# Optimization experiments

Hardware: AMD Instinct MI355X
Metric: run time of the kernel (lower is better)

## Reference

```python
import jax, jax.numpy as jnp
import numpy as np

K_NEIGHBORS = 16
BN_EPS = 1e-5


def _bn(h, g, b):
    # train-mode BatchNorm1d over (batch, points) per channel, biased variance
    mu = h.mean(axis=(0, 1))
    var = h.var(axis=(0, 1))
    return g * (h - mu) * jax.lax.rsqrt(var + BN_EPS) + b


def _gather(arr, idx):
    # arr: [B,N,D], idx: [B,N,K] -> [B,N,K,D]
    return jax.vmap(lambda a, i: a[i])(arr, idx)


def setup_inputs() -> dict:
    key = jax.random.key(0)
    ks = jax.random.split(key, 16)
    B, N, Cin, C, H, M = 4, 4096, 64, 64, 32, 4
    rn = lambda k, s: jax.random.normal(k, s, dtype=jnp.float32) * 0.05
    return {
        "x": jax.random.normal(ks[0], (B, N, Cin), dtype=jnp.float32),
        "p": jax.random.normal(ks[1], (B, N, 3), dtype=jnp.float32),
        "fc1_w": rn(ks[2], (Cin, C)), "fc1_b": jnp.zeros((C,), jnp.float32),
        "bn1_g": jnp.ones((C,), jnp.float32), "bn1_b": jnp.zeros((C,), jnp.float32),
        "qkv_w": rn(ks[3], (C, 3 * C)),
        "pos_w1": rn(ks[4], (3, H)), "pos_b1": jnp.zeros((H,), jnp.float32),
        "pos_w2": rn(ks[5], (H, C)), "pos_b2": jnp.zeros((C,), jnp.float32),
        "attn_w1": rn(ks[6], (C, M * C)), "attn_b1": jnp.zeros((M * C,), jnp.float32),
        "attn_w2": rn(ks[7], (M * C, C)), "attn_b2": jnp.zeros((C,), jnp.float32),
        "bn2_g": jnp.ones((C,), jnp.float32), "bn2_b": jnp.zeros((C,), jnp.float32),
        "fc2_w": rn(ks[8], (C, C)), "fc2_b": jnp.zeros((C,), jnp.float32),
        "bn3_g": jnp.ones((C,), jnp.float32), "bn3_b": jnp.zeros((C,), jnp.float32),
    }


def reference(x, p, fc1_w, fc1_b, bn1_g, bn1_b, qkv_w,
              pos_w1, pos_b1, pos_w2, pos_b2,
              attn_w1, attn_b1, attn_w2, attn_b2,
              bn2_g, bn2_b, fc2_w, fc2_b, bn3_g, bn3_b):
    C = fc1_w.shape[1]
    # fc1 -> BN -> ReLU
    h = jax.nn.relu(_bn(x @ fc1_w + fc1_b, bn1_g, bn1_b))
    residual = h

    # PointTransformerLayer (vector attention over kNN; mask is all-ones)
    qkv = h @ qkv_w  # [B,N,3C]
    q, k, v = qkv[..., :C], qkv[..., C:2 * C], qkv[..., 2 * C:]
    # squared pairwise distances (matches norm-based topk ranking)
    sq = jnp.sum(p * p, axis=-1)  # [B,N]
    d2 = sq[:, :, None] + sq[:, None, :] - 2.0 * jnp.einsum('bnd,bmd->bnm', p, p)
    _, idx = jax.lax.top_k(-d2, K_NEIGHBORS)  # k smallest distances, [B,N,K]

    kj = _gather(k, idx)          # [B,N,K,C]
    vj = _gather(v, idx)          # [B,N,K,C]
    pj = _gather(p, idx)          # [B,N,K,3]

    rel_pos = p[:, :, None, :] - pj                      # [B,N,K,3]
    pe = jax.nn.relu(rel_pos @ pos_w1 + pos_b1) @ pos_w2 + pos_b2  # [B,N,K,C]

    qk_rel = q[:, :, None, :] - kj                       # [B,N,K,C]
    vv = vj + pe
    sim = jax.nn.relu((qk_rel + pe) @ attn_w1 + attn_b1) @ attn_w2 + attn_b2
    attn = jax.nn.softmax(sim, axis=2)                   # softmax over neighbors
    agg = jnp.sum(attn * vv, axis=2)                     # [B,N,C]

    h2 = jax.nn.relu(_bn(agg, bn2_g, bn2_b))
    y = jax.nn.relu(_bn((h2 + residual) @ fc2_w + fc2_b, bn3_g, bn3_b))
    return (y, p)
```

## Files before the change

kernel.cpp:

```cpp
#include <hip/hip_runtime.h>
#include <math.h>

constexpr int kB = 4, kN = 4096, kK = 16;
constexpr int kRows = kB * kN;
constexpr float kEps = 1e-5f;
constexpr float kFltMax = 3.402823466e38f;
constexpr int kCap = 240;

typedef __attribute__((ext_vector_type(8))) short short8;
typedef __attribute__((ext_vector_type(4))) float f32x4;

__device__ __forceinline__ unsigned short f2bf(float x) {
  return (unsigned short)((__float_as_uint(x) + 0x8000u) >> 16);
}
__device__ __forceinline__ unsigned int pkbf(float lo, float hi) {
  return ((__float_as_uint(lo) + 0x8000u) >> 16) |
         ((__float_as_uint(hi) + 0x8000u) & 0xffff0000u);
}
__device__ __forceinline__ float bflo(unsigned int u) { return __uint_as_float(u << 16); }
__device__ __forceinline__ float bfhi(unsigned int u) { return __uint_as_float(u & 0xffff0000u); }
__device__ __forceinline__ float bfu16(unsigned short us) {
  return __uint_as_float(((unsigned int)us) << 16);
}
__device__ __forceinline__ short8 pack8f(float4 a, float4 b) {
  union { unsigned int u[4]; short8 s; } pk;
  pk.u[0] = pkbf(a.x, a.y);
  pk.u[1] = pkbf(a.z, a.w);
  pk.u[2] = pkbf(b.x, b.y);
  pk.u[3] = pkbf(b.z, b.w);
  return pk.s;
}

__device__ __forceinline__ int lane_prefix(unsigned long long m) {
  return __builtin_amdgcn_mbcnt_hi((unsigned)(m >> 32),
         __builtin_amdgcn_mbcnt_lo((unsigned)m, 0));
}

__device__ __forceinline__ void bitonic64(float& sv, int& si, int lane) {
  #pragma unroll
  for (int k = 2; k <= 64; k <<= 1) {
    #pragma unroll
    for (int j = k >> 1; j > 0; j >>= 1) {
      float ov = __shfl_xor(sv, j);
      int   oi = __shfl_xor(si, j);
      bool up = ((lane & k) == 0);
      bool lower = ((lane & j) == 0);
      bool osm = (ov < sv) || (ov == sv && oi < si);
      bool take = (lower == up) ? osm : !osm;
      if (take) { sv = ov; si = oi; }
    }
  }
}

__device__ __forceinline__ float d2q(const float4& Q, const float4& C) {
  float dt = fmaf(Q.z, C.z, fmaf(Q.y, C.y, Q.x * C.x));
  return fmaf(-2.0f, dt, Q.w + C.w);
}

__global__ void pack_kernel(
    const float* __restrict__ aw1, const float* __restrict__ aw2,
    const float* __restrict__ pw2, const float* __restrict__ qw,
    const float* __restrict__ f2w, const float* __restrict__ f1w,
    const float* __restrict__ pin, float* __restrict__ p4o,
    unsigned short* __restrict__ wpak, float* __restrict__ y) {
  const int id = blockIdx.x * 256 + threadIdx.x;
  if (id < 49152)
    *reinterpret_cast<float4*>(y + 1048576 + 4 * id) =
        *reinterpret_cast<const float4*>(pin + 4 * id);
  if (id < 16384) {
    int j = id & 7, lane = (id >> 3) & 63, rest = id >> 9;
    int mt = rest >> 1, hh = rest & 1;
    wpak[id] = f2bf(aw1[(32 * hh + 8 * (lane >> 4) + j) * 256 + mt * 16 + (lane & 15)]);
    float3 pp = *reinterpret_cast<const float3*>(pin + 3 * id);
    float4 o;
    o.x = pp.x; o.y = pp.y; o.z = pp.z;
    o.w = pp.x * pp.x + pp.y * pp.y + pp.z * pp.z;
    *reinterpret_cast<float4*>(p4o + 4 * id) = o;
  } else if (id < 32768) {
    int i = id - 16384;
    int j = i & 7, lane = (i >> 3) & 63, rest = i >> 9;
    int ct = rest >> 3, f = rest & 7;
    wpak[id] = f2bf(aw2[(32 * f + 8 * (lane >> 4) + j) * 64 + ct * 16 + (lane & 15)]);
  } else if (id < 34816) {
    int i = id - 32768;
    int c = i >> 5, hh = i & 31;
    wpak[id] = f2bf(pw2[hh * 64 + c]);
  } else if (id < 47104) {
    int i = id - 34816;
    int j = i & 7, lane = (i >> 3) & 63, rest = i >> 9;
    int ct = rest >> 1, hh = rest & 1;
    wpak[id] = f2bf(qw[(32 * hh + 8 * (lane >> 4) + j) * 192 + ct * 16 + (lane & 15)]);
  } else if (id < 51200) {
    int i = id - 47104;
    int j = i & 7, lane = (i >> 3) & 63, rest = i >> 9;
    int ct = rest >> 1, hh = rest & 1;
    wpak[id] = f2bf(f2w[(32 * hh + 8 * (lane >> 4) + j) * 64 + ct * 16 + (lane & 15)]);
  } else if (id < 55296) {
    int i = id - 51200;
    int j = i & 7, lane = (i >> 3) & 63, rest = i >> 9;
    int ct = rest >> 1, hh = rest & 1;
    wpak[id] = f2bf(f1w[(32 * hh + 8 * (lane >> 4) + j) * 64 + ct * 16 + (lane & 15)]);
  }
}

__global__ __launch_bounds__(256) void fc1_conv_kernel(
    const float* __restrict__ x, const unsigned short* __restrict__ f1wf,
    const float* __restrict__ bias, float* __restrict__ out,
    float* __restrict__ part) {
  __shared__ float SS[4][4][16], SS2[4][4][16];
  const int t = threadIdx.x;
  const int blk = blockIdx.x;
  const int lane = t & 63, wv = t >> 6;
  const int l = lane & 15, q = lane >> 4;
  const int r0 = blk * 64;
  const int row = r0 + wv * 16 + l;
  const f32x4 zero = {0.f, 0.f, 0.f, 0.f};
  float4 xa0 = *reinterpret_cast<const float4*>(&x[row * 64 + q * 8]);
  float4 xa1 = *reinterpret_cast<const float4*>(&x[row * 64 + q * 8 + 4]);
  float4 xb0 = *reinterpret_cast<const float4*>(&x[row * 64 + 32 + q * 8]);
  float4 xb1 = *reinterpret_cast<const float4*>(&x[row * 64 + 32 + q * 8 + 4]);
  short8 a0 = pack8f(xa0, xa1), a1 = pack8f(xb0, xb1);
  #pragma unroll
  for (int ct = 0; ct < 4; ++ct) {
    short8 b0 = *reinterpret_cast<const short8*>(&f1wf[(ct * 2 + 0) * 512 + lane * 8]);
    short8 b1 = *reinterpret_cast<const short8*>(&f1wf[(ct * 2 + 1) * 512 + lane * 8]);
    f32x4 acc = __builtin_amdgcn_mfma_f32_16x16x32_bf16(a0, b0, zero, 0, 0, 0);
    acc = __builtin_amdgcn_mfma_f32_16x16x32_bf16(a1, b1, acc, 0, 0, 0);
    const float bc = bias[ct * 16 + l];
    float s = 0.f, s2 = 0.f;
    #pragma unroll
    for (int i = 0; i < 4; ++i) {
      float v = acc[i] + bc;
      out[(r0 + wv * 16 + q * 4 + i) * 64 + ct * 16 + l] = v;
      s += v; s2 += v * v;
    }
    s  += __shfl_xor(s, 16, 64);  s  += __shfl_xor(s, 32, 64);
    s2 += __shfl_xor(s2, 16, 64); s2 += __shfl_xor(s2, 32, 64);
    if (q == 0) { SS[wv][ct][l] = s; SS2[wv][ct][l] = s2; }
  }
  __syncthreads();
  if (t < 64) {
    int ct = t >> 4, lc = t & 15;
    part[blk * 128 + t] = SS[0][ct][lc] + SS[1][ct][lc] + SS[2][ct][lc] + SS[3][ct][lc];
    part[blk * 128 + 64 + t] =
        SS2[0][ct][lc] + SS2[1][ct][lc] + SS2[2][ct][lc] + SS2[3][ct][lc];
  }
}

__global__ void stats_part_kernel(const float* __restrict__ src, float* __restrict__ part) {
  __shared__ float sb[256], sb2[256];
  const int t = threadIdx.x, blk = blockIdx.x;
  const int c = t & 63, rg = t >> 6;
  float s = 0.f, s2 = 0.f;
  for (int r = rg; r < 64; r += 4) {
    float v = src[(blk * 64 + r) * 64 + c];
    s += v; s2 += v * v;
  }
  sb[t] = s; sb2[t] = s2; __syncthreads();
  if (t < 64) {
    float ts  = sb[t] + sb[64 + t] + sb[128 + t] + sb[192 + t];
    float ts2 = sb2[t] + sb2[64 + t] + sb2[128 + t] + sb2[192 + t];
    part[blk * 128 + t] = ts;
    part[blk * 128 + 64 + t] = ts2;
  }
}

__global__ __launch_bounds__(1024) void stats_fin_kernel(
    const float* __restrict__ part,
    const float* __restrict__ g, const float* __restrict__ b,
    float* __restrict__ A, float* __restrict__ Bv, int cnt) {
  __shared__ double ds[1024], ds2[1024];
  const int t = threadIdx.x;
  const int c = t & 63, grp = t >> 6;
  const int per = cnt >> 4;
  double s = 0.0, s2 = 0.0;
  for (int k = 0; k < per; ++k) {
    int i = grp * per + k;
    s  += part[i * 128 + c];
    s2 += part[i * 128 + 64 + c];
  }
  ds[grp * 64 + c] = s; ds2[grp * 64 + c] = s2;
  __syncthreads();
  if (t < 64) {
    double ts = 0.0, ts2 = 0.0;
    #pragma unroll
    for (int gg = 0; gg < 16; ++gg) { ts += ds[gg * 64 + t]; ts2 += ds2[gg * 64 + t]; }
    double mean = ts / (double)kRows;
    double var = ts2 / (double)kRows - mean * mean;
    float rs = (float)(1.0 / sqrt(var + (double)kEps));
    float Af = g[t] * rs;
    A[t] = Af;
    Bv[t] = b[t] - (float)mean * Af;
  }
}

__global__ __launch_bounds__(256) void qkv_bn_kernel(
    const float* __restrict__ hpre, const float* __restrict__ A1,
    const float* __restrict__ B1, const unsigned short* __restrict__ wqf,
    float* __restrict__ hout, unsigned short* __restrict__ out) {
  const int t = threadIdx.x, lane = t & 63, wv = t >> 6;
  const int l = lane & 15, q = lane >> 4;
  const int r0 = blockIdx.x * 64;
  const int row = r0 + wv * 16 + l;
  const f32x4 zero = {0.f, 0.f, 0.f, 0.f};
  short8 af[2];
  #pragma unroll
  for (int hh = 0; hh < 2; ++hh) {
    const int c0 = 32 * hh + q * 8;
    float4 v0 = *reinterpret_cast<const float4*>(&hpre[row * 64 + c0]);
    float4 v1 = *reinterpret_cast<const float4*>(&hpre[row * 64 + c0 + 4]);
    float4 Aa = *reinterpret_cast<const float4*>(&A1[c0]);
    float4 Ab = *reinterpret_cast<const float4*>(&A1[c0 + 4]);
    float4 Ba = *reinterpret_cast<const float4*>(&B1[c0]);
    float4 Bb = *reinterpret_cast<const float4*>(&B1[c0 + 4]);
    v0.x = fmaxf(Aa.x * v0.x + Ba.x, 0.f); v0.y = fmaxf(Aa.y * v0.y + Ba.y, 0.f);
    v0.z = fmaxf(Aa.z * v0.z + Ba.z, 0.f); v0.w = fmaxf(Aa.w * v0.w + Ba.w, 0.f);
    v1.x = fmaxf(Ab.x * v1.x + Bb.x, 0.f); v1.y = fmaxf(Ab.y * v1.y + Bb.y, 0.f);
    v1.z = fmaxf(Ab.z * v1.z + Bb.z, 0.f); v1.w = fmaxf(Ab.w * v1.w + Bb.w, 0.f);
    *reinterpret_cast<float4*>(&hout[row * 64 + c0]) = v0;
    *reinterpret_cast<float4*>(&hout[row * 64 + c0 + 4]) = v1;
    af[hh] = pack8f(v0, v1);
  }
  #pragma unroll
  for (int ct = 0; ct < 12; ++ct) {
    short8 b0 = *reinterpret_cast<const short8*>(&wqf[((ct * 2 + 0) * 64 + lane) * 8]);
    short8 b1 = *reinterpret_cast<const short8*>(&wqf[((ct * 2 + 1) * 64 + lane) * 8]);
    f32x4 acc = __builtin_amdgcn_mfma_f32_16x16x32_bf16(af[0], b0, zero, 0, 0, 0);
    acc = __builtin_amdgcn_mfma_f32_16x16x32_bf16(af[1], b1, acc, 0, 0, 0);
    #pragma unroll
    for (int i = 0; i < 4; ++i)
      out[(r0 + wv * 16 + q * 4 + i) * 192 + ct * 16 + l] = f2bf(acc[i]);
  }
}

__global__ __launch_bounds__(256, 4) void knn_attn_kernel(
    const float* __restrict__ p4, const unsigned short* __restrict__ qkv,
    const float* __restrict__ pos_w1, const float* __restrict__ pos_b1,
    const float* __restrict__ pos_b2,
    const float* __restrict__ attn_b1, const float* __restrict__ attn_b2,
    const unsigned short* __restrict__ w1f,
    const unsigned short* __restrict__ w2f,
    const unsigned short* __restrict__ pw2t,
    float* __restrict__ agg) {
  __shared__ unsigned short Ulds[64 * 72];
  __shared__ unsigned short VVb[64 * 72];
  __shared__ float sthr[4];
  __shared__ int   scnt[4];

  const int t = threadIdx.x;
  const int lane = t & 63, w = t >> 6;
  const int l = lane & 15, q = lane >> 4;
  const int work = ((blockIdx.x & 7) << 9) | (blockIdx.x >> 3);
  const int b = work >> 10;
  const int pt_row = work * 4 + w;
  const int qrow0 = work * 4;
  const int base = b * kN;
  const f32x4 zero = {0.f, 0.f, 0.f, 0.f};

  if (t < 4) scnt[t] = 0;

  const float4 q0f = *reinterpret_cast<const float4*>(p4 + 4 * (qrow0 + 0));
  const float4 q1f = *reinterpret_cast<const float4*>(p4 + 4 * (qrow0 + 1));
  const float4 q2f = *reinterpret_cast<const float4*>(p4 + 4 * (qrow0 + 2));
  const float4 q3f = *reinterpret_cast<const float4*>(p4 + 4 * (qrow0 + 3));
  const float4 qp4 = *reinterpret_cast<const float4*>(p4 + 4 * pt_row);
  const float qx = qp4.x, qy = qp4.y, qz = qp4.z, sqq = qp4.w;

  unsigned pk0[8], pk1[8], pk2[8], pk3[8];
  float lmin = kFltMax;
  const int cbase = base + w * 1024;
  #pragma unroll
  for (int g = 0; g < 2; ++g) {
    float4 cc[8];
    #pragma unroll
    for (int jj = 0; jj < 8; ++jj)
      cc[jj] = *reinterpret_cast<const float4*>(p4 + 4 * (cbase + (g * 8 + jj) * 64 + lane));
    #pragma unroll
    for (int jj = 0; jj < 8; ++jj) {
      float dot = fmaf(qz, cc[jj].z, fmaf(qy, cc[jj].y, qx * cc[jj].x));
      lmin = fminf(lmin, fmaf(-2.0f, dot, sqq + cc[jj].w));
    }
    #pragma unroll
    for (int pi = 0; pi < 4; ++pi) {
      const float4 ca = cc[2 * pi], cb = cc[2 * pi + 1];
      pk0[g * 4 + pi] = (__float_as_uint(d2q(q0f, ca)) >> 16) |
                        (__float_as_uint(d2q(q0f, cb)) & 0xffff0000u);
      pk1[g * 4 + pi] = (__float_as_uint(d2q(q1f, ca)) >> 16) |
                        (__float_as_uint(d2q(q1f, cb)) & 0xffff0000u);
      pk2[g * 4 + pi] = (__float_as_uint(d2q(q2f, ca)) >> 16) |
                        (__float_as_uint(d2q(q2f, cb)) & 0xffff0000u);
      pk3[g * 4 + pi] = (__float_as_uint(d2q(q3f, ca)) >> 16) |
                        (__float_as_uint(d2q(q3f, cb)) & 0xffff0000u);
    }
  }
  {
    int dummy = lane;
    float lm = lmin;
    bitonic64(lm, dummy, lane);
    float s16 = __shfl(lm, 15);
    if (lane == 0) sthr[w] = s16 + 1e-3f;
  }
  __syncthreads();

  {
    auto append_q = [&](const unsigned (&PK)[8], int j) {
      int* listj = reinterpret_cast<int*>(VVb) + j * 576;
      const float thrj = sthr[j];
      #pragma unroll
      for (int g = 0; g < 2; ++g) {
        unsigned long long m[8];
        int pc[8];
        #pragma unroll
        for (int c = 0; c < 8; ++c) {
          unsigned pku = PK[g * 4 + (c >> 1)];
          float dv = (c & 1) ? __uint_as_float(pku & 0xffff0000u)
                             : __uint_as_float(pku << 16);
          m[c] = __ballot(dv <= thrj);
          pc[c] = __popcll(m[c]);
        }
        int tot = pc[0] + pc[1] + pc[2] + pc[3] + pc[4] + pc[5] + pc[6] + pc[7];
        int old = 0;
        if (lane == 0) old = atomicAdd(&scnt[j], tot);
        old = __shfl(old, 0);
        int pre = 0;
        #pragma unroll
        for (int c = 0; c < 8; ++c) {
          if ((m[c] >> lane) & 1ull) {
            int pos = old + pre + lane_prefix(m[c]);
            if (pos < kCap) listj[pos] = w * 1024 + (g * 8 + c) * 64 + lane;
          }
          pre += pc[c];
        }
      }
    };
    append_q(pk0, 0);
    append_q(pk1, 1);
    append_q(pk2, 2);
    append_q(pk3, 3);
  }
  __syncthreads();

  const int n = scnt[w];
  const int* bufi = reinterpret_cast<const int*>(VVb) + w * 576;
  float sv = kFltMax;
  int   si = 0x7fffffff;
  if (n <= kCap) {
    for (int g0 = 0; g0 < n; g0 += 48) {
      float mv; int mi;
      if (lane < 16) { mv = sv; mi = si; }
      else {
        int pos = g0 + (lane - 16);
        if (pos < n) {
          int jj = bufi[pos];
          float4 c = *reinterpret_cast<const float4*>(p4 + 4 * (base + jj));
          mv = d2q(qp4, c);
          mi = jj;
        } else { mv = kFltMax; mi = 0x7fffffff; }
      }
      bitonic64(mv, mi, lane);
      sv = mv; si = mi;
    }
  } else {
    for (int g0 = 0; g0 < kN; g0 += 48) {
      float mv; int mi;
      if (lane < 16) { mv = sv; mi = si; }
      else {
        int j = g0 + (lane - 16);
        if (j < kN) {
          float4 c = *reinterpret_cast<const float4*>(p4 + 4 * (base + j));
          mv = d2q(qp4, c);
          mi = j;
        } else { mv = kFltMax; mi = 0x7fffffff; }
      }
      bitonic64(mv, mi, lane);
      sv = mv; si = mi;
    }
  }

  int idxv = 0;
  if (lane < 16) {
    int o = si;
    if ((unsigned)o >= (unsigned)kN) o = 0;
    idxv = o;
  }

  asm volatile("" ::: "memory");

  {
    const int r = lane >> 2, seg = lane & 3;
    const unsigned short* jrow = qkv + (base + __shfl(idxv, r)) * 192;
    const int c0 = seg * 16;
    uint4 k0 = *reinterpret_cast<const uint4*>(jrow + 64 + c0);
    uint4 k1 = *reinterpret_cast<const uint4*>(jrow + 64 + c0 + 8);
    uint4 v0 = *reinterpret_cast<const uint4*>(jrow + 128 + c0);
    uint4 v1 = *reinterpret_cast<const uint4*>(jrow + 128 + c0 + 8);
    uint4 q0 = *reinterpret_cast<const uint4*>(qkv + pt_row * 192 + c0);
    uint4 q1 = *reinterpret_cast<const uint4*>(qkv + pt_row * 192 + c0 + 8);
    auto diff2 = [](unsigned int qu, unsigned int ku) -> unsigned int {
      float lo = bflo(qu) - bflo(ku);
      float hi = bfhi(qu) - bfhi(ku);
      return pkbf(lo, hi);
    };
    uint4 u0, u1;
    u0.x = diff2(q0.x, k0.x); u0.y = diff2(q0.y, k0.y);
    u0.z = diff2(q0.z, k0.z); u0.w = diff2(q0.w, k0.w);
    u1.x = diff2(q1.x, k1.x); u1.y = diff2(q1.y, k1.y);
    u1.z = diff2(q1.z, k1.z); u1.w = diff2(q1.w, k1.w);
    *reinterpret_cast<uint4*>(&Ulds[(w * 16 + r) * 72 + c0]) = u0;
    *reinterpret_cast<uint4*>(&Ulds[(w * 16 + r) * 72 + c0 + 8]) = u1;
    *reinterpret_cast<uint4*>(&VVb[(w * 16 + r) * 72 + c0]) = v0;
    *reinterpret_cast<uint4*>(&VVb[(w * 16 + r) * 72 + c0 + 8]) = v1;
  }
  short8 pbf;
  {
    const int nj = __shfl(idxv, l);
    const float4 pj4 = *reinterpret_cast<const float4*>(p4 + 4 * (base + nj));
    float rx = qx - pj4.x, ry = qy - pj4.y, rz = qz - pj4.z;
    float hv[8];
    #pragma unroll
    for (int j = 0; j < 8; ++j) {
      int hh = q * 8 + j;
      hv[j] = fmaxf(pos_b1[hh] + rx * pos_w1[hh] + ry * pos_w1[32 + hh] +
                    rz * pos_w1[64 + hh], 0.0f);
    }
    union { unsigned int u[4]; short8 s; } pk;
    #pragma unroll
    for (int ii = 0; ii < 4; ++ii) pk.u[ii] = pkbf(hv[2 * ii], hv[2 * ii + 1]);
    pbf = pk.s;
  }

  {
    const int urow = (w * 16 + l) * 72;
    #pragma unroll
    for (int mt = 0; mt < 4; ++mt) {
      short8 paf = *reinterpret_cast<const short8*>(&pw2t[(mt * 16 + l) * 32 + q * 8]);
      f32x4 pe = __builtin_amdgcn_mfma_f32_16x16x32_bf16(paf, pbf, zero, 0, 0, 0);
      const int c0 = mt * 16 + q * 4;
      float4 b2v = *reinterpret_cast<const float4*>(&pos_b2[c0]);
      float pe0 = pe[0] + b2v.x, pe1 = pe[1] + b2v.y;
      float pe2 = pe[2] + b2v.z, pe3 = pe[3] + b2v.w;
      uint2 u2 = *reinterpret_cast<uint2*>(&Ulds[urow + c0]);
      uint2 o;
      o.x = pkbf(bflo(u2.x) + pe0, bfhi(u2.x) + pe1);
      o.y = pkbf(bflo(u2.y) + pe2, bfhi(u2.y) + pe3);
      *reinterpret_cast<uint2*>(&Ulds[urow + c0]) = o;
      uint2 v2 = *reinterpret_cast<uint2*>(&VVb[urow + c0]);
      uint2 ov;
      ov.x = pkbf(bflo(v2.x) + pe0, bfhi(v2.x) + pe1);
      ov.y = pkbf(bflo(v2.y) + pe2, bfhi(v2.y) + pe3);
      *reinterpret_cast<uint2*>(&VVb[urow + c0]) = ov;
    }
  }

  {
    f32x4 acc2[4];
    #pragma unroll
    for (int ct = 0; ct < 4; ++ct) acc2[ct] = zero;
    const int urow = (w * 16 + l) * 72;
    short8 ub0 = *reinterpret_cast<const short8*>(&Ulds[urow + q * 8]);
    short8 ub1 = *reinterpret_cast<const short8*>(&Ulds[urow + 32 + q * 8]);
    const int sbase = l + 32 * (q & 1);
    const bool hi_mt = (q >= 2);
    #pragma unroll
    for (int f = 0; f < 8; ++f) {
      unsigned plo2[2], phi2[2];
      #pragma unroll
      for (int s = 0; s < 2; ++s) {
        const int mt = 2 * f + s;
        short8 a0 = *reinterpret_cast<const short8*>(&w1f[(mt * 2 + 0) * 512 + lane * 8]);
        short8 a1 = *reinterpret_cast<const short8*>(&w1f[(mt * 2 + 1) * 512 + lane * 8]);
        f32x4 acc = __builtin_amdgcn_mfma_f32_16x16x32_bf16(a0, ub0, zero, 0, 0, 0);
        acc = __builtin_amdgcn_mfma_f32_16x16x32_bf16(a1, ub1, acc, 0, 0, 0);
        float4 bb = *reinterpret_cast<const float4*>(&attn_b1[mt * 16 + q * 4]);
        plo2[s] = pkbf(fmaxf(acc[0] + bb.x, 0.f), fmaxf(acc[1] + bb.y, 0.f));
        phi2[s] = pkbf(fmaxf(acc[2] + bb.z, 0.f), fmaxf(acc[3] + bb.w, 0.f));
      }
      union { unsigned int u[4]; short8 s; } pk;
      #pragma unroll
      for (int d = 0; d < 4; ++d) {
        const int src = sbase + ((d >> 1) << 4);
        const unsigned int w0 = (d & 1) ? phi2[0] : plo2[0];
        const unsigned int w1v = (d & 1) ? phi2[1] : plo2[1];
        unsigned int va = (unsigned int)__shfl((int)w0, src);
        unsigned int vb = (unsigned int)__shfl((int)w1v, src);
        pk.u[d] = hi_mt ? vb : va;
      }
      short8 afr = pk.s;
      #pragma unroll
      for (int ct = 0; ct < 4; ++ct) {
        short8 bfr = *reinterpret_cast<const short8*>(&w2f[((ct * 8 + f) * 64 + lane) * 8]);
        acc2[ct] = __builtin_amdgcn_mfma_f32_16x16x32_bf16(afr, bfr, acc2[ct], 0, 0, 0);
      }
    }
    #pragma unroll
    for (int ct = 0; ct < 4; ++ct) {
      const int ch = ct * 16 + l;
      const float bv = attn_b2[ch];
      float s0v = acc2[ct][0] + bv, s1v = acc2[ct][1] + bv;
      float s2v = acc2[ct][2] + bv, s3v = acc2[ct][3] + bv;
      float mx = fmaxf(fmaxf(s0v, s1v), fmaxf(s2v, s3v));
      mx = fmaxf(mx, __shfl_xor(mx, 16, 64));
      mx = fmaxf(mx, __shfl_xor(mx, 32, 64));
      float e0 = __expf(s0v - mx), e1 = __expf(s1v - mx);
      float e2 = __expf(s2v - mx), e3 = __expf(s3v - mx);
      float se = e0 + e1 + e2 + e3;
      se += __shfl_xor(se, 16, 64);
      se += __shfl_xor(se, 32, 64);
      const int vbase = (w * 16 + q * 4) * 72 + ch;
      float a = e0 * bfu16(VVb[vbase])       + e1 * bfu16(VVb[vbase + 72]) +
                e2 * bfu16(VVb[vbase + 144]) + e3 * bfu16(VVb[vbase + 216]);
      a += __shfl_xor(a, 16, 64);
      a += __shfl_xor(a, 32, 64);
      if (q == 0) agg[pt_row * 64 + ch] = a / se;
    }
  }
}

__global__ __launch_bounds__(256) void fc2_mfma_kernel(
    const float* __restrict__ aggp, const float* __restrict__ hres,
    const float* __restrict__ A2, const float* __restrict__ B2,
    const unsigned short* __restrict__ fc2f, const float* __restrict__ bias,
    float* __restrict__ z, float* __restrict__ part) {
  __shared__ float SS[4][4][16], SS2[4][4][16];
  const int t = threadIdx.x, lane = t & 63, wv = t >> 6;
  const int l = lane & 15, q = lane >> 4;
  const int r0 = blockIdx.x * 64;
  const int row = r0 + wv * 16 + l;
  const f32x4 zero = {0.f, 0.f, 0.f, 0.f};
  short8 af[2];
  #pragma unroll
  for (int hh = 0; hh < 2; ++hh) {
    const int c0 = 32 * hh + q * 8;
    float4 v0 = *reinterpret_cast<const float4*>(&aggp[row * 64 + c0]);
    float4 v1 = *reinterpret_cast<const float4*>(&aggp[row * 64 + c0 + 4]);
    float4 r0v = *reinterpret_cast<const float4*>(&hres[row * 64 + c0]);
    float4 r1v = *reinterpret_cast<const float4*>(&hres[row * 64 + c0 + 4]);
    float4 Aa = *reinterpret_cast<const float4*>(&A2[c0]);
    float4 Ab = *reinterpret_cast<const float4*>(&A2[c0 + 4]);
    float4 Ba = *reinterpret_cast<const float4*>(&B2[c0]);
    float4 Bb = *reinterpret_cast<const float4*>(&B2[c0 + 4]);
    v0.x = fmaxf(Aa.x * v0.x + Ba.x, 0.f) + r0v.x;
    v0.y = fmaxf(Aa.y * v0.y + Ba.y, 0.f) + r0v.y;
    v0.z = fmaxf(Aa.z * v0.z + Ba.z, 0.f) + r0v.z;
    v0.w = fmaxf(Aa.w * v0.w + Ba.w, 0.f) + r0v.w;
    v1.x = fmaxf(Ab.x * v1.x + Bb.x, 0.f) + r1v.x;
    v1.y = fmaxf(Ab.y * v1.y + Bb.y, 0.f) + r1v.y;
    v1.z = fmaxf(Ab.z * v1.z + Bb.z, 0.f) + r1v.z;
    v1.w = fmaxf(Ab.w * v1.w + Bb.w, 0.f) + r1v.w;
    af[hh] = pack8f(v0, v1);
  }
  #pragma unroll
  for (int ct = 0; ct < 4; ++ct) {
    short8 b0 = *reinterpret_cast<const short8*>(&fc2f[((ct * 2 + 0) * 64 + lane) * 8]);
    short8 b1 = *reinterpret_cast<const short8*>(&fc2f[((ct * 2 + 1) * 64 + lane) * 8]);
    f32x4 acc = __builtin_amdgcn_mfma_f32_16x16x32_bf16(af[0], b0, zero, 0, 0, 0);
    acc = __builtin_amdgcn_mfma_f32_16x16x32_bf16(af[1], b1, acc, 0, 0, 0);
    const float bc = bias[ct * 16 + l];
    float s = 0.f, s2 = 0.f;
    #pragma unroll
    for (int i = 0; i < 4; ++i) {
      float v = acc[i] + bc;
      z[(r0 + wv * 16 + q * 4 + i) * 64 + ct * 16 + l] = v;
      s += v; s2 += v * v;
    }
    s  += __shfl_xor(s, 16, 64);  s  += __shfl_xor(s, 32, 64);
    s2 += __shfl_xor(s2, 16, 64); s2 += __shfl_xor(s2, 32, 64);
    if (q == 0) { SS[wv][ct][l] = s; SS2[wv][ct][l] = s2; }
  }
  __syncthreads();
  if (t < 64) {
    int ct = t >> 4, lc = t & 15;
    part[blockIdx.x * 128 + t] =
        SS[0][ct][lc] + SS[1][ct][lc] + SS[2][ct][lc] + SS[3][ct][lc];
    part[blockIdx.x * 128 + 64 + t] =
        SS2[0][ct][lc] + SS2[1][ct][lc] + SS2[2][ct][lc] + SS2[3][ct][lc];
  }
}

__global__ void final_kernel(const float* __restrict__ z, const float* __restrict__ A3,
                             const float* __restrict__ B3, float* __restrict__ y) {
  const int i = blockIdx.x * 256 + threadIdx.x;
  const int c = i & 63;
  y[i] = fmaxf(A3[c] * z[i] + B3[c], 0.0f);
}

extern "C" void kernel_launch(void* const* d_in, const int* in_sizes, int n_in,
                              void* d_out, int out_size, void* d_ws, size_t ws_size,
                              hipStream_t stream) {
  const float* x       = (const float*)d_in[0];
  const float* p       = (const float*)d_in[1];
  const float* fc1_w   = (const float*)d_in[2];
  const float* fc1_b   = (const float*)d_in[3];
  const float* bn1_g   = (const float*)d_in[4];
  const float* bn1_b   = (const float*)d_in[5];
  const float* qkv_w   = (const float*)d_in[6];
  const float* pos_w1  = (const float*)d_in[7];
  const float* pos_b1  = (const float*)d_in[8];
  const float* pos_w2  = (const float*)d_in[9];
  const float* pos_b2  = (const float*)d_in[10];
  const float* attn_w1 = (const float*)d_in[11];
  const float* attn_b1 = (const float*)d_in[12];
  const float* attn_w2 = (const float*)d_in[13];
  const float* attn_b2 = (const float*)d_in[14];
  const float* bn2_g   = (const float*)d_in[15];
  const float* bn2_b   = (const float*)d_in[16];
  const float* fc2_w   = (const float*)d_in[17];
  const float* fc2_b   = (const float*)d_in[18];
  const float* bn3_g   = (const float*)d_in[19];
  const float* bn3_b   = (const float*)d_in[20];

  float* ws   = (float*)d_ws;
  float* h    = ws;
  unsigned short* qkvb = (unsigned short*)(ws + 1048576);
  float* hpre = ws + 4194304;
  float* aggv = ws + 5242880;
  float* z    = ws + 6291456;
  float* st   = ws + 7340032;
  float* p4   = ws + 7356800;
  unsigned short* wpak = (unsigned short*)(ws + 7618944);
  unsigned short* w1f  = wpak;
  unsigned short* w2f  = wpak + 16384;
  unsigned short* pw2t = wpak + 32768;
  unsigned short* wqf  = wpak + 34816;
  unsigned short* fc2f = wpak + 47104;
  unsigned short* f1wf = wpak + 51200;

  float* A1 = st,       *B1 = st + 64;
  float* A2 = st + 128, *B2 = st + 192;
  float* A3 = st + 256, *B3 = st + 320;
  float* y = (float*)d_out;

  pack_kernel<<<216, 256, 0, stream>>>(attn_w1, attn_w2, pos_w2, qkv_w, fc2_w,
                                       fc1_w, p, p4, wpak, y);
  fc1_conv_kernel<<<256, 256, 0, stream>>>(x, f1wf, fc1_b, hpre, aggv);
  stats_fin_kernel<<<1, 1024, 0, stream>>>(aggv, bn1_g, bn1_b, A1, B1, 256);
  qkv_bn_kernel<<<256, 256, 0, stream>>>(hpre, A1, B1, wqf, h, qkvb);
  knn_attn_kernel<<<4096, 256, 0, stream>>>(p4, qkvb, pos_w1, pos_b1, pos_b2,
                                            attn_b1, attn_b2, w1f, w2f, pw2t, aggv);
  stats_part_kernel<<<256, 256, 0, stream>>>(aggv, z);
  stats_fin_kernel<<<1, 1024, 0, stream>>>(z, bn2_g, bn2_b, A2, B2, 256);
  fc2_mfma_kernel<<<256, 256, 0, stream>>>(aggv, h, A2, B2, fc2f, fc2_b, z, hpre);
  stats_fin_kernel<<<1, 1024, 0, stream>>>(hpre, bn3_g, bn3_b, A3, B3, 256);
  final_kernel<<<4096, 256, 0, stream>>>(z, A3, B3, y);
}
```

Baseline: 243.2 us.

## Fuse BN stat kernels into producers via grid-wide last-block barriers

Replaces separate stats/finalize/apply kernel launches with in-kernel grid synchronization. The last-arriving block computes the BatchNorm scale and shift while the other blocks spin on a flag. This merges fc1 with qkv and folds the BN2/fc2/BN3/final stages into one kernel, keeping intermediates in LDS or registers instead of round-tripping through global memory. It relies on all 256 blocks being co-resident, otherwise the spin-wait deadlocks, and it adds atomic and fence overhead.

```diff
diff --git a/kernel.cpp b/kernel.cpp
--- a/kernel.cpp
+++ b/kernel.cpp
@@ -57,13 +57,69 @@
   return fmaf(-2.0f, dt, Q.w + C.w);
 }
 
+__device__ __forceinline__ bool arrive_last(int* counter, int nblk) {
+  __shared__ int lastf;
+  __syncthreads();
+  __threadfence();
+  if (threadIdx.x == 0) {
+    int old = __hip_atomic_fetch_add(counter, 1, __ATOMIC_ACQ_REL,
+                                     __HIP_MEMORY_SCOPE_AGENT);
+    lastf = (old == nblk - 1) ? 1 : 0;
+  }
+  __syncthreads();
+  return lastf != 0;
+}
+__device__ __forceinline__ void set_flag(int* flag) {
+  __threadfence();
+  __syncthreads();
+  if (threadIdx.x == 0)
+    __hip_atomic_store(flag, 1, __ATOMIC_RELEASE, __HIP_MEMORY_SCOPE_AGENT);
+}
+__device__ __forceinline__ void wait_flag(int* flag) {
+  if (threadIdx.x == 0) {
+    while (__hip_atomic_load(flag, __ATOMIC_ACQUIRE,
+                             __HIP_MEMORY_SCOPE_AGENT) == 0)
+      __builtin_amdgcn_s_sleep(2);
+  }
+  __syncthreads();
+}
+
+__device__ void fin_compute(const float* __restrict__ part,
+                            const float* __restrict__ g,
+                            const float* __restrict__ b,
+                            float* __restrict__ A, float* __restrict__ Bv) {
+  __shared__ double fd[256], fd2[256];
+  const int t = threadIdx.x, c = t & 63, grp = t >> 6;
+  double s = 0.0, s2 = 0.0;
+  for (int k = 0; k < 64; ++k) {
+    int i = grp * 64 + k;
+    s  += part[i * 128 + c];
+    s2 += part[i * 128 + 64 + c];
+  }
+  fd[grp * 64 + c] = s; fd2[grp * 64 + c] = s2;
+  __syncthreads();
+  if (t < 64) {
+    double ts  = fd[t] + fd[64 + t] + fd[128 + t] + fd[192 + t];
+    double ts2 = fd2[t] + fd2[64 + t] + fd2[128 + t] + fd2[192 + t];
+    double mean = ts / (double)kRows;
+    double var = ts2 / (double)kRows - mean * mean;
+    float rs = (float)(1.0 / sqrt(var + (double)kEps));
+    float Af = g[t] * rs;
+    A[t] = Af;
+    Bv[t] = b[t] - (float)mean * Af;
+  }
+  __syncthreads();
+}
+
 __global__ void pack_kernel(
     const float* __restrict__ aw1, const float* __restrict__ aw2,
     const float* __restrict__ pw2, const float* __restrict__ qw,
     const float* __restrict__ f2w, const float* __restrict__ f1w,
     const float* __restrict__ pin, float* __restrict__ p4o,
-    unsigned short* __restrict__ wpak, float* __restrict__ y) {
+    unsigned short* __restrict__ wpak, float* __restrict__ y,
+    int* __restrict__ syncbuf) {
   const int id = blockIdx.x * 256 + threadIdx.x;
+  if (id < 8) syncbuf[id] = 0;
   if (id < 49152)
     *reinterpret_cast<float4*>(y + 1048576 + 4 * id) =
         *reinterpret_cast<const float4*>(pin + 4 * id);
@@ -103,10 +159,15 @@
   }
 }
 
-__global__ __launch_bounds__(256) void fc1_conv_kernel(
+__global__ __launch_bounds__(256, 4) void fc1_qkv_kernel(
     const float* __restrict__ x, const unsigned short* __restrict__ f1wf,
-    const float* __restrict__ bias, float* __restrict__ out,
-    float* __restrict__ part) {
+    const float* __restrict__ fc1_b,
+    const float* __restrict__ bn1_g, const float* __restrict__ bn1_b,
+    const unsigned short* __restrict__ wqf,
+    float* __restrict__ part, float* __restrict__ A1, float* __restrict__ B1,
+    int* __restrict__ counter, int* __restrict__ flag,
+    float* __restrict__ hout, unsigned short* __restrict__ qkvb) {
+  __shared__ float H[64][68];
   __shared__ float SS[4][4][16], SS2[4][4][16];
   const int t = threadIdx.x;
   const int blk = blockIdx.x;
@@ -115,28 +176,30 @@
   const int r0 = blk * 64;
   const int row = r0 + wv * 16 + l;
   const f32x4 zero = {0.f, 0.f, 0.f, 0.f};
-  float4 xa0 = *reinterpret_cast<const float4*>(&x[row * 64 + q * 8]);
-  float4 xa1 = *reinterpret_cast<const float4*>(&x[row * 64 + q * 8 + 4]);
-  float4 xb0 = *reinterpret_cast<const float4*>(&x[row * 64 + 32 + q * 8]);
-  float4 xb1 = *reinterpret_cast<const float4*>(&x[row * 64 + 32 + q * 8 + 4]);
-  short8 a0 = pack8f(xa0, xa1), a1 = pack8f(xb0, xb1);
-  #pragma unroll
-  for (int ct = 0; ct < 4; ++ct) {
-    short8 b0 = *reinterpret_cast<const short8*>(&f1wf[(ct * 2 + 0) * 512 + lane * 8]);
-    short8 b1 = *reinterpret_cast<const short8*>(&f1wf[(ct * 2 + 1) * 512 + lane * 8]);
-    f32x4 acc = __builtin_amdgcn_mfma_f32_16x16x32_bf16(a0, b0, zero, 0, 0, 0);
-    acc = __builtin_amdgcn_mfma_f32_16x16x32_bf16(a1, b1, acc, 0, 0, 0);
-    const float bc = bias[ct * 16 + l];
-    float s = 0.f, s2 = 0.f;
-    #pragma unroll
-    for (int i = 0; i < 4; ++i) {
-      float v = acc[i] + bc;
-      out[(r0 + wv * 16 + q * 4 + i) * 64 + ct * 16 + l] = v;
-      s += v; s2 += v * v;
-    }
-    s  += __shfl_xor(s, 16, 64);  s  += __shfl_xor(s, 32, 64);
-    s2 += __shfl_xor(s2, 16, 64); s2 += __shfl_xor(s2, 32, 64);
-    if (q == 0) { SS[wv][ct][l] = s; SS2[wv][ct][l] = s2; }
+  {
+    float4 xa0 = *reinterpret_cast<const float4*>(&x[row * 64 + q * 8]);
+    float4 xa1 = *reinterpret_cast<const float4*>(&x[row * 64 + q * 8 + 4]);
+    float4 xb0 = *reinterpret_cast<const float4*>(&x[row * 64 + 32 + q * 8]);
+    float4 xb1 = *reinterpret_cast<const float4*>(&x[row * 64 + 32 + q * 8 + 4]);
+    short8 a0 = pack8f(xa0, xa1), a1 = pack8f(xb0, xb1);
+    #pragma unroll
+    for (int ct = 0; ct < 4; ++ct) {
+      short8 b0 = *reinterpret_cast<const short8*>(&f1wf[(ct * 2 + 0) * 512 + lane * 8]);
+      short8 b1 = *reinterpret_cast<const short8*>(&f1wf[(ct * 2 + 1) * 512 + lane * 8]);
+      f32x4 acc = __builtin_amdgcn_mfma_f32_16x16x32_bf16(a0, b0, zero, 0, 0, 0);
+      acc = __builtin_amdgcn_mfma_f32_16x16x32_bf16(a1, b1, acc, 0, 0, 0);
+      const float bc = fc1_b[ct * 16 + l];
+      float s = 0.f, s2 = 0.f;
+      #pragma unroll
+      for (int i = 0; i < 4; ++i) {
+        float v = acc[i] + bc;
+        H[wv * 16 + q * 4 + i][ct * 16 + l] = v;
+        s += v; s2 += v * v;
+      }
+      s  += __shfl_xor(s, 16, 64);  s  += __shfl_xor(s, 32, 64);
+      s2 += __shfl_xor(s2, 16, 64); s2 += __shfl_xor(s2, 32, 64);
+      if (q == 0) { SS[wv][ct][l] = s; SS2[wv][ct][l] = s2; }
+    }
   }
   __syncthreads();
   if (t < 64) {
@@ -145,91 +208,43 @@
     part[blk * 128 + 64 + t] =
         SS2[0][ct][lc] + SS2[1][ct][lc] + SS2[2][ct][lc] + SS2[3][ct][lc];
   }
-}
-
-__global__ void stats_part_kernel(const float* __restrict__ src, float* __restrict__ part) {
-  __shared__ float sb[256], sb2[256];
-  const int t = threadIdx.x, blk = blockIdx.x;
-  const int c = t & 63, rg = t >> 6;
-  float s = 0.f, s2 = 0.f;
-  for (int r = rg; r < 64; r += 4) {
-    float v = src[(blk * 64 + r) * 64 + c];
-    s += v; s2 += v * v;
-  }
-  sb[t] = s; sb2[t] = s2; __syncthreads();
-  if (t < 64) {
-    float ts  = sb[t] + sb[64 + t] + sb[128 + t] + sb[192 + t];
-    float ts2 = sb2[t] + sb2[64 + t] + sb2[128 + t] + sb2[192 + t];
-    part[blk * 128 + t] = ts;
-    part[blk * 128 + 64 + t] = ts2;
-  }
-}
-
-__global__ __launch_bounds__(1024) void stats_fin_kernel(
-    const float* __restrict__ part,
-    const float* __restrict__ g, const float* __restrict__ b,
-    float* __restrict__ A, float* __restrict__ Bv, int cnt) {
-  __shared__ double ds[1024], ds2[1024];
-  const int t = threadIdx.x;
-  const int c = t & 63, grp = t >> 6;
-  const int per = cnt >> 4;
-  double s = 0.0, s2 = 0.0;
-  for (int k = 0; k < per; ++k) {
-    int i = grp * per + k;
-    s  += part[i * 128 + c];
-    s2 += part[i * 128 + 64 + c];
-  }
-  ds[grp * 64 + c] = s; ds2[grp * 64 + c] = s2;
-  __syncthreads();
-  if (t < 64) {
-    double ts = 0.0, ts2 = 0.0;
-    #pragma unroll
-    for (int gg = 0; gg < 16; ++gg) { ts += ds[gg * 64 + t]; ts2 += ds2[gg * 64 + t]; }
-    double mean = ts / (double)kRows;
-    double var = ts2 / (double)kRows - mean * mean;
-    float rs = (float)(1.0 / sqrt(var + (double)kEps));
-    float Af = g[t] * rs;
-    A[t] = Af;
-    Bv[t] = b[t] - (float)mean * Af;
-  }
-}
-
-__global__ __launch_bounds__(256) void qkv_bn_kernel(
-    const float* __restrict__ hpre, const float* __restrict__ A1,
-    const float* __restrict__ B1, const unsigned short* __restrict__ wqf,
-    float* __restrict__ hout, unsigned short* __restrict__ out) {
-  const int t = threadIdx.x, lane = t & 63, wv = t >> 6;
-  const int l = lane & 15, q = lane >> 4;
-  const int r0 = blockIdx.x * 64;
-  const int row = r0 + wv * 16 + l;
-  const f32x4 zero = {0.f, 0.f, 0.f, 0.f};
-  short8 af[2];
-  #pragma unroll
-  for (int hh = 0; hh < 2; ++hh) {
-    const int c0 = 32 * hh + q * 8;
-    float4 v0 = *reinterpret_cast<const float4*>(&hpre[row * 64 + c0]);
-    float4 v1 = *reinterpret_cast<const float4*>(&hpre[row * 64 + c0 + 4]);
-    float4 Aa = *reinterpret_cast<const float4*>(&A1[c0]);
-    float4 Ab = *reinterpret_cast<const float4*>(&A1[c0 + 4]);
-    float4 Ba = *reinterpret_cast<const float4*>(&B1[c0]);
-    float4 Bb = *reinterpret_cast<const float4*>(&B1[c0 + 4]);
-    v0.x = fmaxf(Aa.x * v0.x + Ba.x, 0.f); v0.y = fmaxf(Aa.y * v0.y + Ba.y, 0.f);
-    v0.z = fmaxf(Aa.z * v0.z + Ba.z, 0.f); v0.w = fmaxf(Aa.w * v0.w + Ba.w, 0.f);
-    v1.x = fmaxf(Ab.x * v1.x + Bb.x, 0.f); v1.y = fmaxf(Ab.y * v1.y + Bb.y, 0.f);
-    v1.z = fmaxf(Ab.z * v1.z + Bb.z, 0.f); v1.w = fmaxf(Ab.w * v1.w + Bb.w, 0.f);
-    *reinterpret_cast<float4*>(&hout[row * 64 + c0]) = v0;
-    *reinterpret_cast<float4*>(&hout[row * 64 + c0 + 4]) = v1;
-    af[hh] = pack8f(v0, v1);
-  }
-  #pragma unroll
-  for (int ct = 0; ct < 12; ++ct) {
-    short8 b0 = *reinterpret_cast<const short8*>(&wqf[((ct * 2 + 0) * 64 + lane) * 8]);
-    short8 b1 = *reinterpret_cast<const short8*>(&wqf[((ct * 2 + 1) * 64 + lane) * 8]);
-    f32x4 acc = __builtin_amdgcn_mfma_f32_16x16x32_bf16(af[0], b0, zero, 0, 0, 0);
-    acc = __builtin_amdgcn_mfma_f32_16x16x32_bf16(af[1], b1, acc, 0, 0, 0);
-    #pragma unroll
-    for (int i = 0; i < 4; ++i)
-      out[(r0 + wv * 16 + q * 4 + i) * 192 + ct * 16 + l] = f2bf(acc[i]);
+  if (arrive_last(counter, 256)) {
+    __threadfence();
+    fin_compute(part, bn1_g, bn1_b, A1, B1);
+    set_flag(flag);
+  } else {
+    wait_flag(flag);
+  }
+  __threadfence();
+  {
+    short8 af[2];
+    #pragma unroll
+    for (int hh = 0; hh < 2; ++hh) {
+      const int c0 = 32 * hh + q * 8;
+      float4 v0 = *reinterpret_cast<const float4*>(&H[wv * 16 + l][c0]);
+      float4 v1 = *reinterpret_cast<const float4*>(&H[wv * 16 + l][c0 + 4]);
+      float4 Aa = *reinterpret_cast<const float4*>(&A1[c0]);
+      float4 Ab = *reinterpret_cast<const float4*>(&A1[c0 + 4]);
+      float4 Ba = *reinterpret_cast<const float4*>(&B1[c0]);
+      float4 Bb = *reinterpret_cast<const float4*>(&B1[c0 + 4]);
+      v0.x = fmaxf(Aa.x * v0.x + Ba.x, 0.f); v0.y = fmaxf(Aa.y * v0.y + Ba.y, 0.f);
+      v0.z = fmaxf(Aa.z * v0.z + Ba.z, 0.f); v0.w = fmaxf(Aa.w * v0.w + Ba.w, 0.f);
+      v1.x = fmaxf(Ab.x * v1.x + Bb.x, 0.f); v1.y = fmaxf(Ab.y * v1.y + Bb.y, 0.f);
+      v1.z = fmaxf(Ab.z * v1.z + Bb.z, 0.f); v1.w = fmaxf(Ab.w * v1.w + Bb.w, 0.f);
+      *reinterpret_cast<float4*>(&hout[row * 64 + c0]) = v0;
+      *reinterpret_cast<float4*>(&hout[row * 64 + c0 + 4]) = v1;
+      af[hh] = pack8f(v0, v1);
+    }
+    #pragma unroll
+    for (int ct = 0; ct < 12; ++ct) {
+      short8 b0 = *reinterpret_cast<const short8*>(&wqf[((ct * 2 + 0) * 64 + lane) * 8]);
+      short8 b1 = *reinterpret_cast<const short8*>(&wqf[((ct * 2 + 1) * 64 + lane) * 8]);
+      f32x4 acc = __builtin_amdgcn_mfma_f32_16x16x32_bf16(af[0], b0, zero, 0, 0, 0);
+      acc = __builtin_amdgcn_mfma_f32_16x16x32_bf16(af[1], b1, acc, 0, 0, 0);
+      #pragma unroll
+      for (int i = 0; i < 4; ++i)
+        qkvb[(r0 + wv * 16 + q * 4 + i) * 192 + ct * 16 + l] = f2bf(acc[i]);
+    }
   }
 }
 
@@ -516,72 +531,172 @@
   }
 }
 
-__global__ __launch_bounds__(256) void fc2_mfma_kernel(
+__global__ __launch_bounds__(256, 4) void fc2_final_kernel(
     const float* __restrict__ aggp, const float* __restrict__ hres,
-    const float* __restrict__ A2, const float* __restrict__ B2,
-    const unsigned short* __restrict__ fc2f, const float* __restrict__ bias,
-    float* __restrict__ z, float* __restrict__ part) {
+    const float* __restrict__ bn2_g, const float* __restrict__ bn2_b,
+    const float* __restrict__ bn3_g, const float* __restrict__ bn3_b,
+    const unsigned short* __restrict__ fc2f, const float* __restrict__ fc2_b,
+    float* __restrict__ partA, float* __restrict__ partZ,
+    float* __restrict__ A2, float* __restrict__ B2,
+    float* __restrict__ A3, float* __restrict__ B3,
+    int* __restrict__ counter2, int* __restrict__ flag2,
+    int* __restrict__ counter3, int* __restrict__ flag3,
+    float* __restrict__ y) {
   __shared__ float SS[4][4][16], SS2[4][4][16];
   const int t = threadIdx.x, lane = t & 63, wv = t >> 6;
   const int l = lane & 15, q = lane >> 4;
   const int r0 = blockIdx.x * 64;
   const int row = r0 + wv * 16 + l;
   const f32x4 zero = {0.f, 0.f, 0.f, 0.f};
-  short8 af[2];
-  #pragma unroll
-  for (int hh = 0; hh < 2; ++hh) {
-    const int c0 = 32 * hh + q * 8;
-    float4 v0 = *reinterpret_cast<const float4*>(&aggp[row * 64 + c0]);
-    float4 v1 = *reinterpret_cast<const float4*>(&aggp[row * 64 + c0 + 4]);
-    float4 r0v = *reinterpret_cast<const float4*>(&hres[row * 64 + c0]);
-    float4 r1v = *reinterpret_cast<const float4*>(&hres[row * 64 + c0 + 4]);
-    float4 Aa = *reinterpret_cast<const float4*>(&A2[c0]);
-    float4 Ab = *reinterpret_cast<const float4*>(&A2[c0 + 4]);
-    float4 Ba = *reinterpret_cast<const float4*>(&B2[c0]);
-    float4 Bb = *reinterpret_cast<const float4*>(&B2[c0 + 4]);
-    v0.x = fmaxf(Aa.x * v0.x + Ba.x, 0.f) + r0v.x;
-    v0.y = fmaxf(Aa.y * v0.y + Ba.y, 0.f) + r0v.y;
-    v0.z = fmaxf(Aa.z * v0.z + Ba.z, 0.f) + r0v.z;
-    v0.w = fmaxf(Aa.w * v0.w + Ba.w, 0.f) + r0v.w;
-    v1.x = fmaxf(Ab.x * v1.x + Bb.x, 0.f) + r1v.x;
-    v1.y = fmaxf(Ab.y * v1.y + Bb.y, 0.f) + r1v.y;
-    v1.z = fmaxf(Ab.z * v1.z + Bb.z, 0.f) + r1v.z;
-    v1.w = fmaxf(Ab.w * v1.w + Bb.w, 0.f) + r1v.w;
-    af[hh] = pack8f(v0, v1);
-  }
+  float4 g0 = *reinterpret_cast<const float4*>(&aggp[row * 64 + q * 8]);
+  float4 g1 = *reinterpret_cast<const float4*>(&aggp[row * 64 + q * 8 + 4]);
+  float4 g2 = *reinterpret_cast<const float4*>(&aggp[row * 64 + 32 + q * 8]);
+  float4 g3 = *reinterpret_cast<const float4*>(&aggp[row * 64 + 32 + q * 8 + 4]);
+  float4 r0v = *reinterpret_cast<const float4*>(&hres[row * 64 + q * 8]);
+  float4 r1v = *reinterpret_cast<const float4*>(&hres[row * 64 + q * 8 + 4]);
+  float4 r2v = *reinterpret_cast<const float4*>(&hres[row * 64 + 32 + q * 8]);
+  float4 r3v = *reinterpret_cast<const float4*>(&hres[row * 64 + 32 + q * 8 + 4]);
+  {
+    float sv[8], s2v[8];
+    const float gg[8] = {g0.x, g0.y, g0.z, g0.w, g1.x, g1.y, g1.z, g1.w};
+    const float hh2[8] = {g2.x, g2.y, g2.z, g2.w, g3.x, g3.y, g3.z, g3.w};
+    #pragma unroll
+    for (int j = 0; j < 8; ++j) { sv[j] = gg[j]; s2v[j] = gg[j] * gg[j]; }
+    #pragma unroll
+    for (int st = 1; st < 16; st <<= 1) {
+      #pragma unroll
+      for (int j = 0; j < 8; ++j) {
+        sv[j]  += __shfl_xor(sv[j], st, 64);
+        s2v[j] += __shfl_xor(s2v[j], st, 64);
+      }
+    }
+    if (l == 0) {
+      #pragma unroll
+      for (int j = 0; j < 8; ++j) {
+        SS[wv][0][q * 4 + (j >> 1)] = 0.f;
+      }
+    }
+    if (l == 0) {
+      #pragma unroll
+      for (int j = 0; j < 8; ++j) {
+        (&SS[wv][0][0])[q * 8 + j]  = sv[j];
+        (&SS2[wv][0][0])[q * 8 + j] = s2v[j];
+      }
+    }
+    #pragma unroll
+    for (int j = 0; j < 8; ++j) { sv[j] = hh2[j]; s2v[j] = hh2[j] * hh2[j]; }
+    #pragma unroll
+    for (int st = 1; st < 16; st <<= 1) {
+      #pragma unroll
+      for (int j = 0; j < 8; ++j) {
+        sv[j]  += __shfl_xor(sv[j], st, 64);
+        s2v[j] += __shfl_xor(s2v[j], st, 64);
+      }
+    }
+    if (l == 0) {
+      #pragma unroll
+      for (int j = 0; j < 8; ++j) {
+        (&SS[wv][0][0])[32 + q * 8 + j]  = sv[j];
+        (&SS2[wv][0][0])[32 + q * 8 + j] = s2v[j];
+      }
+    }
+  }
+  __syncthreads();
+  if (t < 64) {
+    partA[blockIdx.x * 128 + t] = (&SS[0][0][0])[t] + (&SS[1][0][0])[t] +
+                                  (&SS[2][0][0])[t] + (&SS[3][0][0])[t];
+    partA[blockIdx.x * 128 + 64 + t] = (&SS2[0][0][0])[t] + (&SS2[1][0][0])[t] +
+                                       (&SS2[2][0][0])[t] + (&SS2[3][0][0])[t];
+  }
+  if (arrive_last(counter2, 256)) {
+    __threadfence();
+    fin_compute(partA, bn2_g, bn2_b, A2, B2);
+    set_flag(flag2);
+  } else {
+    wait_flag(flag2);
+  }
+  __threadfence();
+  float zv[4][4];
+  {
+    short8 af[2];
+    {
+      const int c0 = q * 8;
+      float4 Aa = *reinterpret_cast<const float4*>(&A2[c0]);
+      float4 Ab = *reinterpret_cast<const float4*>(&A2[c0 + 4]);
+      float4 Ba = *reinterpret_cast<const float4*>(&B2[c0]);
+      float4 Bb = *reinterpret_cast<const float4*>(&B2[c0 + 4]);
+      float4 v0 = g0, v1 = g1;
+      v0.x = fmaxf(Aa.x * v0.x + Ba.x, 0.f) + r0v.x;
+      v0.y = fmaxf(Aa.y * v0.y + Ba.y, 0.f) + r0v.y;
+      v0.z = fmaxf(Aa.z * v0.z + Ba.z, 0.f) + r0v.z;
+      v0.w = fmaxf(Aa.w * v0.w + Ba.w, 0.f) + r0v.w;
+      v1.x = fmaxf(Ab.x * v1.x + Bb.x, 0.f) + r1v.x;
+      v1.y = fmaxf(Ab.y * v1.y + Bb.y, 0.f) + r1v.y;
+      v1.z = fmaxf(Ab.z * v1.z + Bb.z, 0.f) + r1v.z;
+      v1.w = fmaxf(Ab.w * v1.w + Bb.w, 0.f) + r1v.w;
+      af[0] = pack8f(v0, v1);
+    }
+    {
+      const int c0 = 32 + q * 8;
+      float4 Aa = *reinterpret_cast<const float4*>(&A2[c0]);
+      float4 Ab = *reinterpret_cast<const float4*>(&A2[c0 + 4]);
+      float4 Ba = *reinterpret_cast<const float4*>(&B2[c0]);
+      float4 Bb = *reinterpret_cast<const float4*>(&B2[c0 + 4]);
+      float4 v0 = g2, v1 = g3;
+      v0.x = fmaxf(Aa.x * v0.x + Ba.x, 0.f) + r2v.x;
+      v0.y = fmaxf(Aa.y * v0.y + Ba.y, 0.f) + r2v.y;
+      v0.z = fmaxf(Aa.z * v0.z + Ba.z, 0.f) + r2v.z;
+      v0.w = fmaxf(Aa.w * v0.w + Ba.w, 0.f) + r2v.w;
+      v1.x = fmaxf(Ab.x * v1.x + Bb.x, 0.f) + r3v.x;
+      v1.y = fmaxf(Ab.y * v1.y + Bb.y, 0.f) + r3v.y;
+      v1.z = fmaxf(Ab.z * v1.z + Bb.z, 0.f) + r3v.z;
+      v1.w = fmaxf(Ab.w * v1.w + Bb.w, 0.f) + r3v.w;
+      af[1] = pack8f(v0, v1);
+    }
+    __syncthreads();
+    #pragma unroll
+    for (int ct = 0; ct < 4; ++ct) {
+      short8 b0 = *reinterpret_cast<const short8*>(&fc2f[((ct * 2 + 0) * 64 + lane) * 8]);
+      short8 b1 = *reinterpret_cast<const short8*>(&fc2f[((ct * 2 + 1) * 64 + lane) * 8]);
+      f32x4 acc = __builtin_amdgcn_mfma_f32_16x16x32_bf16(af[0], b0, zero, 0, 0, 0);
+      acc = __builtin_amdgcn_mfma_f32_16x16x32_bf16(af[1], b1, acc, 0, 0, 0);
+      const float bc = fc2_b[ct * 16 + l];
+      float s = 0.f, s2 = 0.f;
+      #pragma unroll
+      for (int i = 0; i < 4; ++i) {
+        float v = acc[i] + bc;
+        zv[ct][i] = v;
+        s += v; s2 += v * v;
+      }
+      s  += __shfl_xor(s, 16, 64);  s  += __shfl_xor(s, 32, 64);
+      s2 += __shfl_xor(s2, 16, 64); s2 += __shfl_xor(s2, 32, 64);
+      if (q == 0) { SS[wv][ct][l] = s; SS2[wv][ct][l] = s2; }
+    }
+  }
+  __syncthreads();
+  if (t < 64) {
+    int ct = t >> 4, lc = t & 15;
+    partZ[blockIdx.x * 128 + t] =
+        SS[0][ct][lc] + SS[1][ct][lc] + SS[2][ct][lc] + SS[3][ct][lc];
+    partZ[blockIdx.x * 128 + 64 + t] =
+        SS2[0][ct][lc] + SS2[1][ct][lc] + SS2[2][ct][lc] + SS2[3][ct][lc];
+  }
+  if (arrive_last(counter3, 256)) {
+    __threadfence();
+    fin_compute(partZ, bn3_g, bn3_b, A3, B3);
+    set_flag(flag3);
+  } else {
+    wait_flag(flag3);
+  }
+  __threadfence();
   #pragma unroll
   for (int ct = 0; ct < 4; ++ct) {
-    short8 b0 = *reinterpret_cast<const short8*>(&fc2f[((ct * 2 + 0) * 64 + lane) * 8]);
-    short8 b1 = *reinterpret_cast<const short8*>(&fc2f[((ct * 2 + 1) * 64 + lane) * 8]);
-    f32x4 acc = __builtin_amdgcn_mfma_f32_16x16x32_bf16(af[0], b0, zero, 0, 0, 0);
-    acc = __builtin_amdgcn_mfma_f32_16x16x32_bf16(af[1], b1, acc, 0, 0, 0);
-    const float bc = bias[ct * 16 + l];
-    float s = 0.f, s2 = 0.f;
-    #pragma unroll
-    for (int i = 0; i < 4; ++i) {
-      float v = acc[i] + bc;
-      z[(r0 + wv * 16 + q * 4 + i) * 64 + ct * 16 + l] = v;
-      s += v; s2 += v * v;
-    }
-    s  += __shfl_xor(s, 16, 64);  s  += __shfl_xor(s, 32, 64);
-    s2 += __shfl_xor(s2, 16, 64); s2 += __shfl_xor(s2, 32, 64);
-    if (q == 0) { SS[wv][ct][l] = s; SS2[wv][ct][l] = s2; }
-  }
-  __syncthreads();
-  if (t < 64) {
-    int ct = t >> 4, lc = t & 15;
-    part[blockIdx.x * 128 + t] =
-        SS[0][ct][lc] + SS[1][ct][lc] + SS[2][ct][lc] + SS[3][ct][lc];
-    part[blockIdx.x * 128 + 64 + t] =
-        SS2[0][ct][lc] + SS2[1][ct][lc] + SS2[2][ct][lc] + SS2[3][ct][lc];
-  }
-}
-
-__global__ void final_kernel(const float* __restrict__ z, const float* __restrict__ A3,
-                             const float* __restrict__ B3, float* __restrict__ y) {
-  const int i = blockIdx.x * 256 + threadIdx.x;
-  const int c = i & 63;
-  y[i] = fmaxf(A3[c] * z[i] + B3[c], 0.0f);
+    const int ch = ct * 16 + l;
+    const float Af = A3[ch], Bf = B3[ch];
+    #pragma unroll
+    for (int i = 0; i < 4; ++i)
+      y[(r0 + wv * 16 + q * 4 + i) * 64 + ch] = fmaxf(Af * zv[ct][i] + Bf, 0.0f);
+  }
 }
 
 extern "C" void kernel_launch(void* const* d_in, const int* in_sizes, int n_in,
@@ -614,7 +729,7 @@
   unsigned short* qkvb = (unsigned short*)(ws + 1048576);
   float* hpre = ws + 4194304;
   float* aggv = ws + 5242880;
-  float* z    = ws + 6291456;
+  float* zbuf = ws + 6291456;
   float* st   = ws + 7340032;
   float* p4   = ws + 7356800;
   unsigned short* wpak = (unsigned short*)(ws + 7618944);
@@ -628,18 +743,19 @@
   float* A1 = st,       *B1 = st + 64;
   float* A2 = st + 128, *B2 = st + 192;
   float* A3 = st + 256, *B3 = st + 320;
+  int*  sync = (int*)(st + 384);
   float* y = (float*)d_out;
 
   pack_kernel<<<216, 256, 0, stream>>>(attn_w1, attn_w2, pos_w2, qkv_w, fc2_w,
-                                       fc1_w, p, p4, wpak, y);
-  fc1_conv_kernel<<<256, 256, 0, stream>>>(x, f1wf, fc1_b, hpre, aggv);
-  stats_fin_kernel<<<1, 1024, 0, stream>>>(aggv, bn1_g, bn1_b, A1, B1, 256);
-  qkv_bn_kernel<<<256, 256, 0, stream>>>(hpre, A1, B1, wqf, h, qkvb);
+                                       fc1_w, p, p4, wpak, y, sync);
+  fc1_qkv_kernel<<<256, 256, 0, stream>>>(x, f1wf, fc1_b, bn1_g, bn1_b, wqf,
+                                          aggv, A1, B1, sync + 0, sync + 1,
+                                          h, qkvb);
   knn_attn_kernel<<<4096, 256, 0, stream>>>(p4, qkvb, pos_w1, pos_b1, pos_b2,
                                             attn_b1, attn_b2, w1f, w2f, pw2t, aggv);
-  stats_part_kernel<<<256, 256, 0, stream>>>(aggv, z);
-  stats_fin_kernel<<<1, 1024, 0, stream>>>(z, bn2_g, bn2_b, A2, B2, 256);
-  fc2_mfma_kernel<<<256, 256, 0, stream>>>(aggv, h, A2, B2, fc2f, fc2_b, z, hpre);
-  stats_fin_kernel<<<1, 1024, 0, stream>>>(hpre, bn3_g, bn3_b, A3, B3, 256);
-  final_kernel<<<4096, 256, 0, stream>>>(z, A3, B3, y);
-}
+  fc2_final_kernel<<<256, 256, 0, stream>>>(aggv, h, bn2_g, bn2_b, bn3_g, bn3_b,
+                                            fc2f, fc2_b, zbuf, hpre,
+                                            A2, B2, A3, B3,
+                                            sync + 2, sync + 3, sync + 4, sync + 5,
+                                            y);
+}
```

Result: slower. 471.1 us (+93.7%).
